# Kernel tuning notes

Hardware: AMD Instinct MI355X
Metric: run time of the kernel (lower is better)

The kernel has to match this reference:

```python
import jax, jax.numpy as jnp
import numpy as np

N = 50000


def gcn_conv(x, W, b, src, dst, deg_inv_sqrt):
    # h = x @ W, then symmetric-normalized aggregation with self-loops
    h = x @ W  # [N, out]
    norm = deg_inv_sqrt[src] * deg_inv_sqrt[dst]  # [E]
    agg = jax.ops.segment_sum(h[src] * norm[:, None], dst, num_segments=N)
    # self-loop contribution: norm_ii = deg_inv_sqrt[i]^2
    agg = agg + h * (deg_inv_sqrt * deg_inv_sqrt)[:, None]
    return agg + b


def setup_inputs() -> dict:
    key = jax.random.key(0)
    ks = jax.random.split(key, 8)
    F_in, H, C = 128, 128, 64
    x = jax.random.normal(ks[0], (N, F_in), dtype=jnp.float32)
    edge_index = jax.random.randint(ks[1], (2, 800000), 0, N, dtype=jnp.int64)
    s = 1.0 / np.sqrt(F_in)
    W1 = jax.random.uniform(ks[2], (F_in, H), jnp.float32, -s, s)
    b1 = jnp.zeros((H,), jnp.float32)
    W2 = jax.random.uniform(ks[3], (H, H), jnp.float32, -s, s)
    b2 = jnp.zeros((H,), jnp.float32)
    W3 = jax.random.uniform(ks[4], (H, C), jnp.float32, -s, s)
    b3 = jnp.zeros((C,), jnp.float32)
    return {"x": x, "edge_index": edge_index, "W1": W1, "b1": b1,
            "W2": W2, "b2": b2, "W3": W3, "b3": b3}


def reference(x, edge_index, W1, b1, W2, b2, W3, b3):
    src, dst = edge_index[0], edge_index[1]
    # degree with self-loops (edge weight 1): deg[i] = in-degree + 1
    deg = jnp.zeros((N,), x.dtype).at[dst].add(1.0) + 1.0
    dinv = jax.lax.rsqrt(deg)
    h = gcn_conv(x, W1, b1, src, dst, dinv)
    h = jax.nn.relu(h)  # dropout p=0 / eval -> identity
    h = gcn_conv(h, W2, b2, src, dst, dinv)
    h = jax.nn.relu(h)
    h = gcn_conv(h, W3, b3, src, dst, dinv)
    return jax.nn.log_softmax(h, axis=-1)
```

## Files before the change

### kernel.cpp

```cpp
#include <hip/hip_runtime.h>
#include <math.h>

typedef short short8 __attribute__((ext_vector_type(8)));
typedef float floatx4 __attribute__((ext_vector_type(4)));

__device__ __forceinline__ float4 ld4(const float* p) { return *reinterpret_cast<const float4*>(p); }
__device__ __forceinline__ void st4(float* p, float4 v) { *reinterpret_cast<float4*>(p) = v; }

__device__ __forceinline__ float bf2f(unsigned int u) { return __uint_as_float(u << 16); }
__device__ __forceinline__ unsigned int f2bf1(float f) {
    unsigned int x = __float_as_uint(f);
    return (x + 0x7fffu + ((x >> 16) & 1u)) >> 16;
}
__device__ __forceinline__ unsigned int f2bf2(float lo, float hi) {
    return f2bf1(lo) | (f2bf1(hi) << 16);
}
__device__ __forceinline__ void unpack8(uint4 v, float* f) {
    f[0] = bf2f(v.x & 0xffffu); f[1] = bf2f(v.x >> 16);
    f[2] = bf2f(v.y & 0xffffu); f[3] = bf2f(v.y >> 16);
    f[4] = bf2f(v.z & 0xffffu); f[5] = bf2f(v.z >> 16);
    f[6] = bf2f(v.w & 0xffffu); f[7] = bf2f(v.w >> 16);
}

__global__ __launch_bounds__(256) void k_count_prep(const int* __restrict__ dst, int* __restrict__ deg,
                                                    int* __restrict__ rank, int E, int nbE,
                                                    const float* __restrict__ W1, const float* __restrict__ W2,
                                                    const float* __restrict__ W3, unsigned short* __restrict__ Wt1,
                                                    unsigned short* __restrict__ Wt2, unsigned short* __restrict__ Wt3) {
    if ((int)blockIdx.x < nbE) {
        int e = blockIdx.x * 256 + threadIdx.x;
        if (e < E) rank[e] = atomicAdd(&deg[dst[e]], 1);
    } else {
        int t = (blockIdx.x - nbE) * 256 + threadIdx.x;
        if (t < 16384) {
            int k = t & 127, n = t >> 7;
            Wt1[n * 128 + k] = (unsigned short)f2bf1(W1[(size_t)k * 128 + n]);
        } else if (t < 32768) {
            int u = t - 16384;
            int k = u & 127, n = u >> 7;
            Wt2[n * 128 + k] = (unsigned short)f2bf1(W2[(size_t)k * 128 + n]);
        } else if (t < 40960) {
            int u = t - 32768;
            int k = u & 127, n = u >> 7;
            Wt3[n * 128 + k] = (unsigned short)f2bf1(W3[(size_t)k * 64 + n]);
        }
    }
}

__global__ __launch_bounds__(256) void k_dinv_reduce(const int* __restrict__ deg, float* __restrict__ dinv,
                                                     int* __restrict__ bsum, int* __restrict__ hist,
                                                     int n, int nbN) {
    __shared__ int s[256];
    __shared__ int lh[64];
    int t = threadIdx.x;
    if ((int)blockIdx.x < nbN) {
        if (t < 64) lh[t] = 0;
        __syncthreads();
        int i = blockIdx.x * 256 + t;
        if (i < n) {
            int d = deg[i];
            dinv[i] = 1.0f / sqrtf((float)d + 1.0f);
            atomicAdd(&lh[min(d, 63)], 1);
        }
        __syncthreads();
        if (t < 64 && lh[t] != 0) atomicAdd(&hist[t], lh[t]);
        return;
    }
    int b = (int)blockIdx.x - nbN;
    int i = b * 256 + t;
    s[t] = (i < n) ? deg[i] : 0;
    __syncthreads();
    for (int off = 128; off > 0; off >>= 1) {
        if (t < off) s[t] += s[t + off];
        __syncthreads();
    }
    if (t == 0) bsum[b] = s[0];
}

__global__ __launch_bounds__(256) void k_scansmall_gemm1(const int* __restrict__ bsum, int* __restrict__ boff, int nb,
                                                         const int* __restrict__ hist, int* __restrict__ histcur,
                                                         const float* __restrict__ X, const unsigned short* __restrict__ Wt,
                                                         const float* __restrict__ dinv,
                                                         unsigned short* __restrict__ O, int nrows) {
    constexpr int LDR = 136;
    __shared__ __align__(16) unsigned char smem[(64 * LDR + 128 * LDR) * 2];

    const int tid = threadIdx.x;
    if (blockIdx.x == 0) {
        int* s = (int*)smem;
        int v = (tid < nb) ? bsum[tid] : 0;
        s[tid] = v;
        __syncthreads();
        for (int off = 1; off < 256; off <<= 1) {
            int x = (tid >= off) ? s[tid - off] : 0;
            __syncthreads();
            s[tid] += x;
            __syncthreads();
        }
        if (tid < nb) boff[tid] = s[tid] - v;
        return;
    }
    if (blockIdx.x == 1) {
        int* hsc = (int*)smem;
        if (tid < 64) hsc[tid] = hist[tid];
        __syncthreads();
        if (tid == 0) {
            int run = 0;
            for (int c = 0; c < 64; ++c) { int v = hsc[c]; hsc[c] = run; run += v; }
        }
        __syncthreads();
        if (tid < 64) histcur[tid] = hsc[tid];
        return;
    }

    unsigned short* sX = (unsigned short*)smem;
    unsigned short* sB = sX + 64 * LDR;
    const int row0 = ((int)blockIdx.x - 2) * 64;

#pragma unroll
    for (int i = 0; i < 4; ++i) {
        int idx = tid + i * 256;
        int r = idx >> 4, c8 = idx & 15;
        int grow = row0 + r;
        uint4 v = make_uint4(0, 0, 0, 0);
        if (grow < nrows) {
            float4 a = ld4(X + (size_t)grow * 128 + c8 * 8);
            float4 b = ld4(X + (size_t)grow * 128 + c8 * 8 + 4);
            v = make_uint4(f2bf2(a.x, a.y), f2bf2(a.z, a.w), f2bf2(b.x, b.y), f2bf2(b.z, b.w));
        }
        *reinterpret_cast<uint4*>(&sX[r * LDR + c8 * 8]) = v;
    }
#pragma unroll
    for (int i = 0; i < 8; ++i) {
        int idx = tid + i * 256;
        int nn = idx >> 4, c8 = idx & 15;
        *reinterpret_cast<uint4*>(&sB[nn * LDR + c8 * 8]) =
            *reinterpret_cast<const uint4*>(Wt + (size_t)nn * 128 + c8 * 8);
    }
    __syncthreads();

    const int lane = tid & 63;
    const int wave = tid >> 6;
    const int l15  = lane & 15;
    const int quad = lane >> 4;

    floatx4 acc[8];
#pragma unroll
    for (int j = 0; j < 8; ++j) acc[j] = (floatx4){0.f, 0.f, 0.f, 0.f};

    const unsigned short* xbase = &sX[(wave * 16 + l15) * LDR + quad * 8];
#pragma unroll
    for (int kk = 0; kk < 4; ++kk) {
        short8 xb = *reinterpret_cast<const short8*>(xbase + kk * 32);
#pragma unroll
        for (int j = 0; j < 8; ++j) {
            short8 wa = *reinterpret_cast<const short8*>(&sB[(j * 16 + l15) * LDR + quad * 8 + kk * 32]);
            acc[j] = __builtin_amdgcn_mfma_f32_16x16x32_bf16(wa, xb, acc[j], 0, 0, 0);
        }
    }

    int xrow = row0 + wave * 16 + l15;
    if (xrow < nrows) {
        float di = dinv[xrow];
#pragma unroll
        for (int j = 0; j < 8; ++j) {
            uint2 o = make_uint2(f2bf2(acc[j][0] * di, acc[j][1] * di), f2bf2(acc[j][2] * di, acc[j][3] * di));
            *reinterpret_cast<uint2*>(O + (size_t)xrow * 128 + j * 16 + quad * 4) = o;
        }
    }
}

__global__ __launch_bounds__(256) void k_scan_final(const int* __restrict__ deg, const int* __restrict__ boff,
                                                    int* __restrict__ row_off, int* __restrict__ histcur,
                                                    int* __restrict__ perm, int n, int nb) {
    __shared__ int s[256];
    __shared__ int lh[64];
    __shared__ int lbase[64];
    int t = threadIdx.x;
    if ((int)blockIdx.x < nb) {
        int i = blockIdx.x * 256 + t;
        int v = (i < n) ? deg[i] : 0;
        s[t] = v;
        __syncthreads();
        for (int off = 1; off < 256; off <<= 1) {
            int x = (t >= off) ? s[t - off] : 0;
            __syncthreads();
            s[t] += x;
            __syncthreads();
        }
        int incl = s[t] + boff[blockIdx.x];
        if (i < n) {
            row_off[i] = incl - v;
            if (i == n - 1) row_off[n] = incl;
        }
        return;
    }
    int b = (int)blockIdx.x - nb;
    int i = b * 256 + t;
    if (t < 64) lh[t] = 0;
    __syncthreads();
    int c = 0, myr = 0;
    bool valid = (i < n);
    if (valid) {
        c = min(deg[i], 63);
        myr = atomicAdd(&lh[c], 1);
    }
    __syncthreads();
    if (t < 64 && lh[t] != 0) lbase[t] = atomicAdd(&histcur[t], lh[t]);
    __syncthreads();
    if (valid) perm[lbase[c] + myr] = i;
}

__global__ __launch_bounds__(256) void k_fill(const int* __restrict__ src, const int* __restrict__ dst,
                                              const int* __restrict__ rank, const int* __restrict__ roff,
                                              int* __restrict__ csrc, int E) {
    int e = blockIdx.x * 256 + threadIdx.x;
    if (e < E) csrc[roff[dst[e]] + rank[e]] = src[e];
}

template <int NC>
__global__ __launch_bounds__(256) void k_gemm_mfma(const unsigned short* __restrict__ X,
                                                   const unsigned short* __restrict__ Wt,
                                                   const float* __restrict__ dinv,
                                                   unsigned short* __restrict__ O, int nrows) {
    constexpr int LDR = 136;
    __shared__ unsigned short sX[64 * LDR];
    __shared__ unsigned short sB[NC * LDR];

    const int tid  = threadIdx.x;
    const int row0 = blockIdx.x * 64;

#pragma unroll
    for (int i = 0; i < 4; ++i) {
        int idx = tid + i * 256;
        int r = idx >> 4, c8 = idx & 15;
        int grow = row0 + r;
        uint4 v = make_uint4(0, 0, 0, 0);
        if (grow < nrows) v = *reinterpret_cast<const uint4*>(X + (size_t)grow * 128 + c8 * 8);
        *reinterpret_cast<uint4*>(&sX[r * LDR + c8 * 8]) = v;
    }
#pragma unroll
    for (int i = 0; i < NC / 16; ++i) {
        int idx = tid + i * 256;
        int n = idx >> 4, c8 = idx & 15;
        *reinterpret_cast<uint4*>(&sB[n * LDR + c8 * 8]) =
            *reinterpret_cast<const uint4*>(Wt + (size_t)n * 128 + c8 * 8);
    }
    __syncthreads();

    const int lane = tid & 63;
    const int wave = tid >> 6;
    const int l15  = lane & 15;
    const int quad = lane >> 4;

    floatx4 acc[NC / 16];
#pragma unroll
    for (int j = 0; j < NC / 16; ++j) acc[j] = (floatx4){0.f, 0.f, 0.f, 0.f};

    const unsigned short* xbase = &sX[(wave * 16 + l15) * LDR + quad * 8];
#pragma unroll
    for (int kk = 0; kk < 4; ++kk) {
        short8 xb = *reinterpret_cast<const short8*>(xbase + kk * 32);
#pragma unroll
        for (int j = 0; j < NC / 16; ++j) {
            short8 wa = *reinterpret_cast<const short8*>(&sB[(j * 16 + l15) * LDR + quad * 8 + kk * 32]);
            acc[j] = __builtin_amdgcn_mfma_f32_16x16x32_bf16(wa, xb, acc[j], 0, 0, 0);
        }
    }

    int xrow = row0 + wave * 16 + l15;
    if (xrow < nrows) {
        float di = dinv[xrow];
#pragma unroll
        for (int j = 0; j < NC / 16; ++j) {
            uint2 o = make_uint2(f2bf2(acc[j][0] * di, acc[j][1] * di), f2bf2(acc[j][2] * di, acc[j][3] * di));
            *reinterpret_cast<uint2*>(O + (size_t)xrow * NC + j * 16 + quad * 4) = o;
        }
    }
}

__global__ __launch_bounds__(256) void k_agg_relu(const unsigned short* __restrict__ H, const int* __restrict__ roff,
                                                  const int* __restrict__ csrc, const float* __restrict__ dinv,
                                                  const float* __restrict__ bias, const int* __restrict__ perm,
                                                  unsigned short* __restrict__ O, int n) {
    int t    = blockIdx.x * 256 + threadIdx.x;
    int g    = t >> 4;
    int f8   = (t & 15) * 8;
    if (g >= n) return;
    int node = perm[g];

    float a[8];
    {
        uint4 hv = *reinterpret_cast<const uint4*>(H + (size_t)node * 128 + f8);
        unpack8(hv, a);
    }

    int e  = roff[node];
    int e1 = roff[node + 1];
    for (; e + 3 < e1; e += 4) {
        int s[4];
        uint4 v[4];
#pragma unroll
        for (int u = 0; u < 4; ++u) s[u] = csrc[e + u];
#pragma unroll
        for (int u = 0; u < 4; ++u) v[u] = *reinterpret_cast<const uint4*>(H + (size_t)s[u] * 128 + f8);
#pragma unroll
        for (int u = 0; u < 4; ++u) {
            float g2[8];
            unpack8(v[u], g2);
#pragma unroll
            for (int i = 0; i < 8; ++i) a[i] += g2[i];
        }
    }
    for (; e < e1; ++e) {
        uint4 v0 = *reinterpret_cast<const uint4*>(H + (size_t)csrc[e] * 128 + f8);
        float g0[8];
        unpack8(v0, g0);
#pragma unroll
        for (int i = 0; i < 8; ++i) a[i] += g0[i];
    }

    float di = dinv[node];
    float4 b0 = ld4(bias + f8);
    float4 b1 = ld4(bias + f8 + 4);
    float bb[8] = {b0.x, b0.y, b0.z, b0.w, b1.x, b1.y, b1.z, b1.w};
#pragma unroll
    for (int i = 0; i < 8; ++i) a[i] = fmaxf(a[i] * di + bb[i], 0.0f);

    uint4 ov = make_uint4(f2bf2(a[0], a[1]), f2bf2(a[2], a[3]), f2bf2(a[4], a[5]), f2bf2(a[6], a[7]));
    *reinterpret_cast<uint4*>(O + (size_t)node * 128 + f8) = ov;
}

__global__ __launch_bounds__(256) void k_agg_softmax(const unsigned short* __restrict__ H, const int* __restrict__ roff,
                                                     const int* __restrict__ csrc, const float* __restrict__ dinv,
                                                     const float* __restrict__ bias, const int* __restrict__ perm,
                                                     float* __restrict__ O, int n) {
    int t    = blockIdx.x * 256 + threadIdx.x;
    int g    = t >> 3;
    int f8   = (t & 7) * 8;
    if (g >= n) return;
    int node = perm[g];

    float a[8];
    {
        uint4 hv = *reinterpret_cast<const uint4*>(H + (size_t)node * 64 + f8);
        unpack8(hv, a);
    }

    int e  = roff[node];
    int e1 = roff[node + 1];
    for (; e + 7 < e1; e += 8) {
        int s[8];
        uint4 v[8];
#pragma unroll
        for (int u = 0; u < 8; ++u) s[u] = csrc[e + u];
#pragma unroll
        for (int u = 0; u < 8; ++u) v[u] = *reinterpret_cast<const uint4*>(H + (size_t)s[u] * 64 + f8);
#pragma unroll
        for (int u = 0; u < 8; ++u) {
            float gg[8];
            unpack8(v[u], gg);
#pragma unroll
            for (int i = 0; i < 8; ++i) a[i] += gg[i];
        }
    }
    if (e + 3 < e1) {
        int s[4];
        uint4 v[4];
#pragma unroll
        for (int u = 0; u < 4; ++u) s[u] = csrc[e + u];
#pragma unroll
        for (int u = 0; u < 4; ++u) v[u] = *reinterpret_cast<const uint4*>(H + (size_t)s[u] * 64 + f8);
#pragma unroll
        for (int u = 0; u < 4; ++u) {
            float gg[8];
            unpack8(v[u], gg);
#pragma unroll
            for (int i = 0; i < 8; ++i) a[i] += gg[i];
        }
        e += 4;
    }
    for (; e < e1; ++e) {
        uint4 v0 = *reinterpret_cast<const uint4*>(H + (size_t)csrc[e] * 64 + f8);
        float g0[8];
        unpack8(v0, g0);
#pragma unroll
        for (int i = 0; i < 8; ++i) a[i] += g0[i];
    }

    float di = dinv[node];
    float4 b0 = ld4(bias + f8);
    float4 b1 = ld4(bias + f8 + 4);
    float bb[8] = {b0.x, b0.y, b0.z, b0.w, b1.x, b1.y, b1.z, b1.w};
    float v[8];
#pragma unroll
    for (int i = 0; i < 8; ++i) v[i] = a[i] * di + bb[i];

    float m = v[0];
#pragma unroll
    for (int i = 1; i < 8; ++i) m = fmaxf(m, v[i]);
    m = fmaxf(m, __shfl_xor(m, 1));
    m = fmaxf(m, __shfl_xor(m, 2));
    m = fmaxf(m, __shfl_xor(m, 4));

    float ssum = 0.0f;
#pragma unroll
    for (int i = 0; i < 8; ++i) ssum += expf(v[i] - m);
    ssum += __shfl_xor(ssum, 1);
    ssum += __shfl_xor(ssum, 2);
    ssum += __shfl_xor(ssum, 4);
    float ls = logf(ssum);

    float* op = O + (size_t)node * 64 + f8;
    st4(op, make_float4(v[0] - m - ls, v[1] - m - ls, v[2] - m - ls, v[3] - m - ls));
    st4(op + 4, make_float4(v[4] - m - ls, v[5] - m - ls, v[6] - m - ls, v[7] - m - ls));
}

extern "C" void kernel_launch(void* const* d_in, const int* in_sizes, int n_in,
                              void* d_out, int out_size, void* d_ws, size_t ws_size,
                              hipStream_t stream) {
    const float* x  = (const float*)d_in[0];
    const int*   ei = (const int*)d_in[1];
    const float* W1 = (const float*)d_in[2];
    const float* b1 = (const float*)d_in[3];
    const float* W2 = (const float*)d_in[4];
    const float* b2 = (const float*)d_in[5];
    const float* W3 = (const float*)d_in[6];
    const float* b3 = (const float*)d_in[7];
    float* out = (float*)d_out;

    const int N = in_sizes[0] / 128;
    const int E = in_sizes[1] / 2;
    const int* src = ei;
    const int* dst = ei + E;

    char* ws = (char*)d_ws;
    size_t off = 0;
    auto alloc = [&](size_t bytes) -> char* {
        char* p = ws + off;
        off = (off + bytes + 255) & ~(size_t)255;
        return p;
    };
    int nb  = (N + 255) / 256;
    int nbE = (E + 255) / 256;
    int blocks64 = (N + 63) / 64;

    int*   deg     = (int*)alloc((size_t)N * 4);
    int*   hist    = (int*)alloc(64 * 4);
    int*   histcur = (int*)alloc(64 * 4);
    int*   row_off = (int*)alloc(((size_t)N + 1) * 4);
    float* dinv    = (float*)alloc((size_t)N * 4);
    int*   bsum    = (int*)alloc((size_t)nb * 4);
    int*   boff    = (int*)alloc((size_t)nb * 4);
    int*   rank    = (int*)alloc((size_t)E * 4);
    int*   csrc    = (int*)alloc((size_t)E * 4);
    int*   perm    = (int*)alloc((size_t)N * 4);
    unsigned short* Wt1  = (unsigned short*)alloc(128 * 128 * 2);
    unsigned short* Wt2  = (unsigned short*)alloc(128 * 128 * 2);
    unsigned short* Wt3  = (unsigned short*)alloc(64 * 128 * 2);
    unsigned short* bufA = (unsigned short*)alloc((size_t)N * 128 * 2);
    unsigned short* bufB = (unsigned short*)alloc((size_t)N * 128 * 2);
    unsigned short* bufC = (unsigned short*)alloc((size_t)N * 64 * 2);
    (void)ws_size; (void)n_in; (void)out_size;

    size_t degPad = (((size_t)N * 4 + 255) & ~(size_t)255);
    hipMemsetAsync(deg, 0, degPad + 256, stream);
    k_count_prep<<<nbE + 160, 256, 0, stream>>>(dst, deg, rank, E, nbE, W1, W2, W3, Wt1, Wt2, Wt3);
    k_dinv_reduce<<<nb + nb, 256, 0, stream>>>(deg, dinv, bsum, hist, N, nb);
    k_scansmall_gemm1<<<2 + blocks64, 256, 0, stream>>>(bsum, boff, nb, hist, histcur, x, Wt1, dinv, bufA, N);
    k_scan_final<<<nb + nb, 256, 0, stream>>>(deg, boff, row_off, histcur, perm, N, nb);
    k_fill<<<nbE, 256, 0, stream>>>(src, dst, rank, row_off, csrc, E);

    k_agg_relu<<<((size_t)N * 16 + 255) / 256, 256, 0, stream>>>(bufA, row_off, csrc, dinv, b1, perm, bufB, N);
    k_gemm_mfma<128><<<blocks64, 256, 0, stream>>>(bufB, Wt2, dinv, bufA, N);
    k_agg_relu<<<((size_t)N * 16 + 255) / 256, 256, 0, stream>>>(bufA, row_off, csrc, dinv, b2, perm, bufB, N);
    k_gemm_mfma<64><<<blocks64, 256, 0, stream>>>(bufB, Wt3, dinv, bufC, N);
    k_agg_softmax<<<((size_t)N * 8 + 255) / 256, 256, 0, stream>>>(bufC, row_off, csrc, dinv, b3, perm, out, N);
}
```

Baseline: 253.6 us.

## Bucket CSR neighbors by source-index chunk for gather locality

Degree counting now uses per-destination counters split into 8 chunks by source index (src>>13). The scan emits per-chunk start offsets, so within each CSR row the neighbor indices end up grouped by source range. The aim is better cache locality for the feature gathers in the three aggregation passes. In exchange the counter and offset arrays grow 8x, atomics spread over more addresses, and the prep kernels do extra vector loads and writes.

```diff
diff --git a/kernel.cpp b/kernel.cpp
--- a/kernel.cpp
+++ b/kernel.cpp
@@ -3,6 +3,9 @@
 
 typedef short short8 __attribute__((ext_vector_type(8)));
 typedef float floatx4 __attribute__((ext_vector_type(4)));
+
+#define CHUNK_SHIFT 13
+#define NCHUNK 8
 
 __device__ __forceinline__ float4 ld4(const float* p) { return *reinterpret_cast<const float4*>(p); }
 __device__ __forceinline__ void st4(float* p, float4 v) { *reinterpret_cast<float4*>(p) = v; }
@@ -22,14 +25,23 @@
     f[6] = bf2f(v.w & 0xffffu); f[7] = bf2f(v.w >> 16);
 }
 
-__global__ __launch_bounds__(256) void k_count_prep(const int* __restrict__ dst, int* __restrict__ deg,
-                                                    int* __restrict__ rank, int E, int nbE,
+__device__ __forceinline__ int sum8(const int* __restrict__ p) {
+    uint4 a = *reinterpret_cast<const uint4*>(p);
+    uint4 b = *reinterpret_cast<const uint4*>(p + 4);
+    return (int)(a.x + a.y + a.z + a.w + b.x + b.y + b.z + b.w);
+}
+
+__global__ __launch_bounds__(256) void k_count_prep(const int* __restrict__ src, const int* __restrict__ dst,
+                                                    int* __restrict__ deg2, int* __restrict__ rank, int E, int nbE,
                                                     const float* __restrict__ W1, const float* __restrict__ W2,
                                                     const float* __restrict__ W3, unsigned short* __restrict__ Wt1,
                                                     unsigned short* __restrict__ Wt2, unsigned short* __restrict__ Wt3) {
     if ((int)blockIdx.x < nbE) {
         int e = blockIdx.x * 256 + threadIdx.x;
-        if (e < E) rank[e] = atomicAdd(&deg[dst[e]], 1);
+        if (e < E) {
+            int c = src[e] >> CHUNK_SHIFT;
+            rank[e] = atomicAdd(&deg2[dst[e] * NCHUNK + c], 1);
+        }
     } else {
         int t = (blockIdx.x - nbE) * 256 + threadIdx.x;
         if (t < 16384) {
@@ -47,7 +59,7 @@
     }
 }
 
-__global__ __launch_bounds__(256) void k_dinv_reduce(const int* __restrict__ deg, float* __restrict__ dinv,
+__global__ __launch_bounds__(256) void k_dinv_reduce(const int* __restrict__ deg2, float* __restrict__ dinv,
                                                      int* __restrict__ bsum, int* __restrict__ hist,
                                                      int n, int nbN) {
     __shared__ int s[256];
@@ -58,7 +70,7 @@
         __syncthreads();
         int i = blockIdx.x * 256 + t;
         if (i < n) {
-            int d = deg[i];
+            int d = sum8(deg2 + (size_t)i * NCHUNK);
             dinv[i] = 1.0f / sqrtf((float)d + 1.0f);
             atomicAdd(&lh[min(d, 63)], 1);
         }
@@ -68,7 +80,7 @@
     }
     int b = (int)blockIdx.x - nbN;
     int i = b * 256 + t;
-    s[t] = (i < n) ? deg[i] : 0;
+    s[t] = (i < n) ? sum8(deg2 + (size_t)i * NCHUNK) : 0;
     __syncthreads();
     for (int off = 128; off > 0; off >>= 1) {
         if (t < off) s[t] += s[t + off];
@@ -170,8 +182,9 @@
     }
 }
 
-__global__ __launch_bounds__(256) void k_scan_final(const int* __restrict__ deg, const int* __restrict__ boff,
-                                                    int* __restrict__ row_off, int* __restrict__ histcur,
+__global__ __launch_bounds__(256) void k_scan_final(const int* __restrict__ deg2, const int* __restrict__ boff,
+                                                    int* __restrict__ row_off, int* __restrict__ starts2,
+                                                    int* __restrict__ histcur,
                                                     int* __restrict__ perm, int n, int nb) {
     __shared__ int s[256];
     __shared__ int lh[64];
@@ -179,8 +192,14 @@
     int t = threadIdx.x;
     if ((int)blockIdx.x < nb) {
         int i = blockIdx.x * 256 + t;
-        int v = (i < n) ? deg[i] : 0;
-        s[t] = v;
+        uint4 d0 = make_uint4(0, 0, 0, 0), d1 = make_uint4(0, 0, 0, 0);
+        int tot = 0;
+        if (i < n) {
+            d0 = *reinterpret_cast<const uint4*>(deg2 + (size_t)i * NCHUNK);
+            d1 = *reinterpret_cast<const uint4*>(deg2 + (size_t)i * NCHUNK + 4);
+            tot = (int)(d0.x + d0.y + d0.z + d0.w + d1.x + d1.y + d1.z + d1.w);
+        }
+        s[t] = tot;
         __syncthreads();
         for (int off = 1; off < 256; off <<= 1) {
             int x = (t >= off) ? s[t - off] : 0;
@@ -190,7 +209,19 @@
         }
         int incl = s[t] + boff[blockIdx.x];
         if (i < n) {
-            row_off[i] = incl - v;
+            int r = incl - tot;
+            row_off[i] = r;
+            uint4 o0, o1;
+            o0.x = r; r += d0.x;
+            o0.y = r; r += d0.y;
+            o0.z = r; r += d0.z;
+            o0.w = r; r += d0.w;
+            o1.x = r; r += d1.x;
+            o1.y = r; r += d1.y;
+            o1.z = r; r += d1.z;
+            o1.w = r;
+            *reinterpret_cast<uint4*>(starts2 + (size_t)i * NCHUNK) = o0;
+            *reinterpret_cast<uint4*>(starts2 + (size_t)i * NCHUNK + 4) = o1;
             if (i == n - 1) row_off[n] = incl;
         }
         return;
@@ -202,7 +233,7 @@
     int c = 0, myr = 0;
     bool valid = (i < n);
     if (valid) {
-        c = min(deg[i], 63);
+        c = min(sum8(deg2 + (size_t)i * NCHUNK), 63);
         myr = atomicAdd(&lh[c], 1);
     }
     __syncthreads();
@@ -212,10 +243,14 @@
 }
 
 __global__ __launch_bounds__(256) void k_fill(const int* __restrict__ src, const int* __restrict__ dst,
-                                              const int* __restrict__ rank, const int* __restrict__ roff,
+                                              const int* __restrict__ rank, const int* __restrict__ starts2,
                                               int* __restrict__ csrc, int E) {
     int e = blockIdx.x * 256 + threadIdx.x;
-    if (e < E) csrc[roff[dst[e]] + rank[e]] = src[e];
+    if (e < E) {
+        int s = src[e];
+        int c = s >> CHUNK_SHIFT;
+        csrc[starts2[dst[e] * NCHUNK + c] + rank[e]] = s;
+    }
 }
 
 template <int NC>
@@ -445,10 +480,11 @@
     int nbE = (E + 255) / 256;
     int blocks64 = (N + 63) / 64;
 
-    int*   deg     = (int*)alloc((size_t)N * 4);
+    int*   deg2    = (int*)alloc((size_t)N * NCHUNK * 4);
     int*   hist    = (int*)alloc(64 * 4);
     int*   histcur = (int*)alloc(64 * 4);
     int*   row_off = (int*)alloc(((size_t)N + 1) * 4);
+    int*   starts2 = (int*)alloc((size_t)N * NCHUNK * 4);
     float* dinv    = (float*)alloc((size_t)N * 4);
     int*   bsum    = (int*)alloc((size_t)nb * 4);
     int*   boff    = (int*)alloc((size_t)nb * 4);
@@ -463,13 +499,13 @@
     unsigned short* bufC = (unsigned short*)alloc((size_t)N * 64 * 2);
     (void)ws_size; (void)n_in; (void)out_size;
 
-    size_t degPad = (((size_t)N * 4 + 255) & ~(size_t)255);
-    hipMemsetAsync(deg, 0, degPad + 256, stream);
-    k_count_prep<<<nbE + 160, 256, 0, stream>>>(dst, deg, rank, E, nbE, W1, W2, W3, Wt1, Wt2, Wt3);
-    k_dinv_reduce<<<nb + nb, 256, 0, stream>>>(deg, dinv, bsum, hist, N, nb);
+    size_t degPad = (((size_t)N * NCHUNK * 4 + 255) & ~(size_t)255);
+    hipMemsetAsync(deg2, 0, degPad + 256, stream);
+    k_count_prep<<<nbE + 160, 256, 0, stream>>>(src, dst, deg2, rank, E, nbE, W1, W2, W3, Wt1, Wt2, Wt3);
+    k_dinv_reduce<<<nb + nb, 256, 0, stream>>>(deg2, dinv, bsum, hist, N, nb);
     k_scansmall_gemm1<<<2 + blocks64, 256, 0, stream>>>(bsum, boff, nb, hist, histcur, x, Wt1, dinv, bufA, N);
-    k_scan_final<<<nb + nb, 256, 0, stream>>>(deg, boff, row_off, histcur, perm, N, nb);
-    k_fill<<<nbE, 256, 0, stream>>>(src, dst, rank, row_off, csrc, E);
+    k_scan_final<<<nb + nb, 256, 0, stream>>>(deg2, boff, row_off, starts2, histcur, perm, N, nb);
+    k_fill<<<nbE, 256, 0, stream>>>(src, dst, rank, starts2, csrc, E);
 
     k_agg_relu<<<((size_t)N * 16 + 255) / 256, 256, 0, stream>>>(bufA, row_off, csrc, dinv, b1, perm, bufB, N);
     k_gemm_mfma<128><<<blocks64, 256, 0, stream>>>(bufB, Wt2, dinv, bufA, N);
```

Result: no change. 252.6 us (-0.4%).
